# Kernel optimization log

Measured on AMD Instinct MI355X. Metric: run time of the kernel, lower is better.

The kernel has to match this reference:

```python
import jax, jax.numpy as jnp
import numpy as np
from functools import partial

D = 1024
H = 4 * D
E = 8
K_TOP = 2
B, T = 4, 2048
NEG_INF = jnp.float32(-1e30)


def setup_inputs() -> dict:
    key = jax.random.key(0)
    ks = jax.random.split(key, 12)
    s = 0.02
    return {
        "x": jax.random.normal(ks[0], (B, T, D), jnp.float32),
        "noise": jax.random.normal(ks[1], (B, T, E), jnp.float32),
        "gate_w": jax.random.normal(ks[2], (E, D), jnp.float32) * s,
        "gate_b": jnp.zeros((E,), jnp.float32),
        "var_w": jax.random.normal(ks[3], (E, D), jnp.float32) * s,
        "var_b": jnp.zeros((E,), jnp.float32),
        "w1": jax.random.normal(ks[4], (E, H, D), jnp.float32) * s,
        "b1": jnp.zeros((E, H), jnp.float32),
        "w2": jax.random.normal(ks[5], (E, D, H), jnp.float32) * s,
        "b2": jnp.zeros((E, D), jnp.float32),
    }


def reference(x, noise, gate_w, gate_b, var_w, var_b, w1, b1, w2, b2):
    # Noisy top-k gating
    logits = jnp.einsum("btd,ed->bte", x, gate_w) + gate_b          # [B,T,E]
    std = jax.nn.softplus(jnp.einsum("btd,ed->bte", x, var_w) + var_b)
    noisy = logits + noise * std                                      # [B,T,E]
    _, idx = jax.lax.top_k(noisy, K_TOP)                              # [B,T,K]
    # boolean top-k mask over experts
    mask = (idx[..., None] == jnp.arange(E)).any(axis=-2)             # [B,T,E]
    coef = jax.nn.softmax(jnp.where(mask, noisy, NEG_INF), axis=-1)   # zeros outside top-k

    # Combine: sum_e coef_e * FFN_e(x). coef is exactly 0 for non-selected
    # experts, so this equals the masked gather/scatter math. Scan over the
    # small expert dim to avoid a [E,B,T,H] intermediate.
    coef_e = jnp.moveaxis(coef, -1, 0)                                # [E,B,T]

    def body(acc, ew):
        w1e, b1e, w2e, b2e, ce = ew
        h = jax.nn.relu(jnp.einsum("btd,hd->bth", x, w1e) + b1e)
        y = jnp.einsum("bth,dh->btd", h, w2e) + b2e
        return acc + y * ce[..., None], None

    out, _ = jax.lax.scan(body, jnp.zeros_like(x), (w1, b1, w2, b2, coef_e))
    return out
```

## Files before the change

kernel.cpp:

```cpp
#include <hip/hip_runtime.h>
#include <hip/hip_bf16.h>
#include <math.h>

#define NTOK 8192
#define DD   1024
#define HH   4096
#define NE   8
#define BM 128
#define BN 128
#define BK 64
#define SLOT_CAP (2 * NTOK + NE * BM)

typedef __bf16 bf16;
typedef __bf16 bf16x8 __attribute__((ext_vector_type(8)));
typedef __bf16 bf16x4 __attribute__((ext_vector_type(4)));
typedef float  f32x4  __attribute__((ext_vector_type(4)));

typedef __attribute__((address_space(3))) unsigned char lds_u8;
typedef const __attribute__((address_space(1))) unsigned char g_u8;

__device__ __forceinline__ void gload16(const bf16* g, bf16* l) {
  __builtin_amdgcn_global_load_lds((g_u8*)g, (lds_u8*)l, 16, 0, 0);
}

__device__ __forceinline__ float softplus_f(float v) {
  return fmaxf(v, 0.f) + log1pf(expf(-fabsf(v)));
}

__global__ __launch_bounds__(64) void moe_gate_kernel(
    const float* __restrict__ x, const float* __restrict__ noise,
    const float* __restrict__ gate_w, const float* __restrict__ gate_b,
    const float* __restrict__ var_w,  const float* __restrict__ var_b,
    float* __restrict__ coef2, int* __restrict__ t2e, int* __restrict__ counts,
    bf16* __restrict__ xb)
{
  const int t = blockIdx.x;
  const int lane = threadIdx.x;
  const float* xt = x + (size_t)t * DD;
  bf16* xbt = xb + (size_t)t * DD;
  float pg[NE], pv[NE];
  #pragma unroll
  for (int e = 0; e < NE; ++e) { pg[e] = 0.f; pv[e] = 0.f; }
  #pragma unroll 4
  for (int i = 0; i < DD / 64; ++i) {
    const int d = lane + i * 64;
    const float xv = xt[d];
    xbt[d] = (bf16)xv;
    #pragma unroll
    for (int e = 0; e < NE; ++e) {
      pg[e] = fmaf(xv, gate_w[e * DD + d], pg[e]);
      pv[e] = fmaf(xv, var_w[e * DD + d], pv[e]);
    }
  }
  #pragma unroll
  for (int e = 0; e < NE; ++e) {
    #pragma unroll
    for (int off = 32; off; off >>= 1) {
      pg[e] += __shfl_xor(pg[e], off);
      pv[e] += __shfl_xor(pv[e], off);
    }
  }
  if (lane == 0) {
    float noisy[NE];
    #pragma unroll
    for (int e = 0; e < NE; ++e) {
      const float lg = pg[e] + gate_b[e];
      const float sd = softplus_f(pv[e] + var_b[e]);
      noisy[e] = lg + noise[t * NE + e] * sd;
    }
    int i1 = 0; float n1 = noisy[0];
    #pragma unroll
    for (int e = 1; e < NE; ++e) if (noisy[e] > n1) { n1 = noisy[e]; i1 = e; }
    int i2 = -1; float n2 = -3.0e38f;
    #pragma unroll
    for (int e = 0; e < NE; ++e) if (e != i1 && noisy[e] > n2) { n2 = noisy[e]; i2 = e; }
    const float e2 = expf(n2 - n1);
    const float den = 1.f + e2;
    coef2[t * 2 + 0] = 1.f / den;
    coef2[t * 2 + 1] = e2 / den;
    t2e[t * 2 + 0] = i1;
    t2e[t * 2 + 1] = i2;
    atomicAdd(&counts[i1], 1);
    atomicAdd(&counts[i2], 1);
  }
}

__global__ void moe_offsets_kernel(const int* __restrict__ counts, int* __restrict__ po) {
  if (threadIdx.x == 0) {
    int acc = 0;
    po[0] = 0;
    for (int e = 0; e < NE; ++e) {
      acc += ((counts[e] + BM - 1) / BM) * BM;
      po[e + 1] = acc;
    }
  }
}

__global__ __launch_bounds__(256) void moe_scatter_kernel(
    const int* __restrict__ t2e, const float* __restrict__ coef2,
    const int* __restrict__ po, int* __restrict__ cnt2,
    int* __restrict__ assign_tok, float* __restrict__ slot_coef)
{
  const int t = blockIdx.x * 256 + threadIdx.x;
  if (t >= NTOK) return;
  #pragma unroll
  for (int k = 0; k < 2; ++k) {
    const int e = t2e[t * 2 + k];
    const int pos = atomicAdd(&cnt2[e], 1);
    const int slot = po[e] + pos;
    assign_tok[slot] = t;
    slot_coef[slot] = coef2[t * 2 + k];
  }
}

__global__ __launch_bounds__(256) void cvt_bf16_kernel(const float* __restrict__ src,
                                                       bf16* __restrict__ dst, int n4) {
  for (int i = blockIdx.x * 256 + threadIdx.x; i < n4; i += gridDim.x * 256) {
    const float4 f = ((const float4*)src)[i];
    bf16x4 v;
    v[0] = (bf16)f.x; v[1] = (bf16)f.y; v[2] = (bf16)f.z; v[3] = (bf16)f.w;
    ((bf16x4*)dst)[i] = v;
  }
}

template<int KDIM, int NCOLS, bool FFN1>
__global__ __launch_bounds__(256) void moe_gemm_kernel(
    const bf16* __restrict__ Asrc, const bf16* __restrict__ Wsrc,
    const float* __restrict__ bias,
    const int* __restrict__ assign_tok, const float* __restrict__ slot_coef,
    const int* __restrict__ po,
    bf16* __restrict__ hout, float* __restrict__ out,
    int chunk_base, int gx)
{
  __shared__ bf16 As[BM][BK];
  __shared__ bf16 Bs[BN][BK];
  __shared__ int toks[BM];

  const int nwg = gridDim.x;
  const int lin = blockIdx.x;
  const int q = nwg >> 3, r = nwg & 7;
  const int xcd = lin & 7, idx = lin >> 3;
  const int wg = (xcd < r ? xcd * (q + 1) : r * (q + 1) + (xcd - r) * q) + idx;
  int bx, by;
  if constexpr (FFN1) { bx = wg % gx; by = wg / gx; }
  else               { by = wg % (NCOLS / BN); bx = wg / (NCOLS / BN); }

  const int po8 = po[NE];
  const int row0 = chunk_base + bx * BM;
  if (row0 >= po8) return;
  int e = 0;
  while (row0 >= po[e + 1]) ++e;
  const int bn0 = by * BN;
  const bf16* We = Wsrc + (size_t)e * ((size_t)HH * DD);
  const int tid = threadIdx.x, lane = tid & 63, wave = tid >> 6;
  if (tid < BM) toks[tid] = assign_tok[row0 + tid];
  __syncthreads();

  const int rin = lane >> 3;
  const int c8s = ((lane & 7) ^ rin) * 8;
  const bf16* asrc[4];
  const bf16* bsrc[4];
  #pragma unroll
  for (int i = 0; i < 4; ++i) {
    const int c = wave * 4 + i;
    const int row = c * 8 + rin;
    int ar;
    if constexpr (FFN1) {
      const int s = toks[row];
      ar = s < 0 ? 0 : s;
    } else {
      ar = row0 - chunk_base + row;
    }
    asrc[i] = Asrc + (size_t)ar * KDIM + c8s;
    bsrc[i] = We + (size_t)(bn0 + row) * KDIM + c8s;
  }

  const int la = lane & 15, hi = lane >> 4;
  const int wm = (wave >> 1) * 64, wn = (wave & 1) * 64;
  f32x4 acc[4][4];
  #pragma unroll
  for (int m = 0; m < 4; ++m)
    #pragma unroll
    for (int n = 0; n < 4; ++n) acc[m][n] = {0.f, 0.f, 0.f, 0.f};

  for (int k0 = 0; k0 < KDIM; k0 += BK) {
    #pragma unroll
    for (int i = 0; i < 4; ++i) gload16(asrc[i] + k0, &As[(wave * 4 + i) * 8][0]);
    #pragma unroll
    for (int i = 0; i < 4; ++i) gload16(bsrc[i] + k0, &Bs[(wave * 4 + i) * 8][0]);
    __syncthreads();
    #pragma unroll
    for (int ks = 0; ks < 2; ++ks) {
      bf16x8 af[4], bff[4];
      #pragma unroll
      for (int m = 0; m < 4; ++m) {
        const int row = wm + m * 16 + la;
        const int c8 = (ks * 4 + hi) ^ (row & 7);
        af[m] = *(const bf16x8*)(&As[row][c8 * 8]);
      }
      #pragma unroll
      for (int n = 0; n < 4; ++n) {
        const int row = wn + n * 16 + la;
        const int c8 = (ks * 4 + hi) ^ (row & 7);
        bff[n] = *(const bf16x8*)(&Bs[row][c8 * 8]);
      }
      #pragma unroll
      for (int m = 0; m < 4; ++m)
        #pragma unroll
        for (int n = 0; n < 4; ++n)
          acc[m][n] = __builtin_amdgcn_mfma_f32_16x16x32_bf16(af[m], bff[n], acc[m][n], 0, 0, 0);
    }
    __syncthreads();
  }

  if constexpr (FFN1) {
    const int hrow0 = row0 - chunk_base;
    #pragma unroll
    for (int n = 0; n < 4; ++n) {
      const int col = bn0 + wn + n * 16 + la;
      const float bb = bias[e * NCOLS + col];
      #pragma unroll
      for (int m = 0; m < 4; ++m) {
        const int rbase = wm + m * 16 + hi * 4;
        #pragma unroll
        for (int rr = 0; rr < 4; ++rr) {
          float v = acc[m][n][rr] + bb;
          v = v > 0.f ? v : 0.f;
          hout[(size_t)(hrow0 + rbase + rr) * HH + col] = (bf16)v;
        }
      }
    }
  } else {
    #pragma unroll
    for (int n = 0; n < 4; ++n) {
      const int col = bn0 + wn + n * 16 + la;
      const float bb = bias[e * NCOLS + col];
      #pragma unroll
      for (int m = 0; m < 4; ++m) {
        const int rbase = wm + m * 16 + hi * 4;
        #pragma unroll
        for (int rr = 0; rr < 4; ++rr) {
          const int trow = rbase + rr;
          const int tok = toks[trow];
          if (tok >= 0) {
            const float c = slot_coef[row0 + trow];
            atomicAdd(out + (size_t)tok * DD + col, c * (acc[m][n][rr] + bb));
          }
        }
      }
    }
  }
}

extern "C" void kernel_launch(void* const* d_in, const int* in_sizes, int n_in,
                              void* d_out, int out_size, void* d_ws, size_t ws_size,
                              hipStream_t stream) {
  const float* x      = (const float*)d_in[0];
  const float* noise  = (const float*)d_in[1];
  const float* gate_w = (const float*)d_in[2];
  const float* gate_b = (const float*)d_in[3];
  const float* var_w  = (const float*)d_in[4];
  const float* var_b  = (const float*)d_in[5];
  const float* w1     = (const float*)d_in[6];
  const float* b1     = (const float*)d_in[7];
  const float* w2     = (const float*)d_in[8];
  const float* b2     = (const float*)d_in[9];
  float* out = (float*)d_out;
  (void)in_sizes; (void)n_in; (void)out_size;

  char* ws = (char*)d_ws;
  size_t off = 0;
  auto alloc = [&](size_t bytes) {
    off = (off + 255) & ~(size_t)255;
    size_t o = off;
    off += bytes;
    return o;
  };
  bf16*  xb         = (bf16*)(ws + alloc((size_t)NTOK * DD * 2));
  float* coef2      = (float*)(ws + alloc((size_t)NTOK * 2 * 4));
  int*   t2e        = (int*)(ws + alloc((size_t)NTOK * 2 * 4));
  int*   counts     = (int*)(ws + alloc(64));
  int*   cnt2       = counts + 8;
  int*   po         = (int*)(ws + alloc(64));
  int*   assign_tok = (int*)(ws + alloc((size_t)SLOT_CAP * 4));
  float* slot_coef  = (float*)(ws + alloc((size_t)SLOT_CAP * 4));
  bf16*  w1b        = (bf16*)(ws + alloc((size_t)NE * HH * DD * 2));
  bf16*  w2b        = (bf16*)(ws + alloc((size_t)NE * DD * HH * 2));
  off = (off + 255) & ~(size_t)255;
  const size_t h_avail = ws_size > off ? ws_size - off : 0;
  int chunk_rows = (int)(h_avail / ((size_t)HH * 2));
  chunk_rows = (chunk_rows / BM) * BM;
  if (chunk_rows < BM) chunk_rows = BM;
  if (chunk_rows > SLOT_CAP) chunk_rows = SLOT_CAP;
  bf16* hbuf = (bf16*)(ws + off);

  hipMemsetAsync(counts, 0, 64, stream);
  hipMemsetAsync(assign_tok, 0xFF, (size_t)SLOT_CAP * 4, stream);
  hipMemsetAsync(out, 0, (size_t)NTOK * DD * 4, stream);

  moe_gate_kernel<<<NTOK, 64, 0, stream>>>(x, noise, gate_w, gate_b, var_w, var_b,
                                           coef2, t2e, counts, xb);
  moe_offsets_kernel<<<1, 64, 0, stream>>>(counts, po);
  moe_scatter_kernel<<<NTOK / 256, 256, 0, stream>>>(t2e, coef2, po, cnt2,
                                                     assign_tok, slot_coef);
  cvt_bf16_kernel<<<2048, 256, 0, stream>>>(w1, w1b, NE * HH * DD / 4);
  cvt_bf16_kernel<<<2048, 256, 0, stream>>>(w2, w2b, NE * DD * HH / 4);

  const int rounds = (SLOT_CAP + chunk_rows - 1) / chunk_rows;
  for (int r = 0; r < rounds; ++r) {
    const int cb = r * chunk_rows;
    const int rows_here = (cb + chunk_rows <= SLOT_CAP) ? chunk_rows : (SLOT_CAP - cb);
    const int gx = rows_here / BM;
    moe_gemm_kernel<DD, HH, true><<<gx * (HH / BN), 256, 0, stream>>>(
        xb, w1b, b1, assign_tok, slot_coef, po, hbuf, nullptr, cb, gx);
    moe_gemm_kernel<HH, DD, false><<<gx * (DD / BN), 256, 0, stream>>>(
        hbuf, w2b, b2, assign_tok, slot_coef, po, nullptr, out, cb, gx);
  }
}
```

Measured before the change: 956.6 us.

## Double-buffer LDS tiles in MoE GEMM and merge weight conversion kernels

The GEMM main loop now keeps two LDS buffers and issues the global-to-LDS loads for the next K tile before computing the current one. It waits with explicit vmcnt counters and raw barriers instead of __syncthreads, so global load latency can overlap the MFMA work. The two fp32-to-bf16 weight conversion launches are also merged into one kernel. In exchange, LDS use per block doubles, which may lower occupancy, and the hand-written waitcnt values depend on each thread having exactly 8 loads in flight per stage.

```diff
diff --git a/kernel.cpp b/kernel.cpp
--- a/kernel.cpp
+++ b/kernel.cpp
@@ -113,15 +113,23 @@
   }
 }
 
-__global__ __launch_bounds__(256) void cvt_bf16_kernel(const float* __restrict__ src,
-                                                       bf16* __restrict__ dst, int n4) {
-  for (int i = blockIdx.x * 256 + threadIdx.x; i < n4; i += gridDim.x * 256) {
-    const float4 f = ((const float4*)src)[i];
+__global__ __launch_bounds__(256) void cvt2_bf16_kernel(
+    const float* __restrict__ s1, bf16* __restrict__ d1, int n41,
+    const float* __restrict__ s2, bf16* __restrict__ d2, int n42)
+{
+  for (int i = blockIdx.x * 256 + threadIdx.x; i < n41 + n42; i += gridDim.x * 256) {
+    const float* s = (i < n41) ? s1 : s2;
+    bf16* d = (i < n41) ? d1 : d2;
+    const int j = (i < n41) ? i : i - n41;
+    const float4 f = ((const float4*)s)[j];
     bf16x4 v;
     v[0] = (bf16)f.x; v[1] = (bf16)f.y; v[2] = (bf16)f.z; v[3] = (bf16)f.w;
-    ((bf16x4*)dst)[i] = v;
-  }
-}
+    ((bf16x4*)d)[j] = v;
+  }
+}
+
+#define VMCNT8 asm volatile("s_waitcnt vmcnt(8)" ::: "memory")
+#define VMCNT0 asm volatile("s_waitcnt vmcnt(0)" ::: "memory")
 
 template<int KDIM, int NCOLS, bool FFN1>
 __global__ __launch_bounds__(256) void moe_gemm_kernel(
@@ -132,8 +140,9 @@
     bf16* __restrict__ hout, float* __restrict__ out,
     int chunk_base, int gx)
 {
-  __shared__ bf16 As[BM][BK];
-  __shared__ bf16 Bs[BN][BK];
+  constexpr int NK = KDIM / BK;
+  __shared__ bf16 As[2][BM][BK];
+  __shared__ bf16 Bs[2][BN][BK];
   __shared__ int toks[BM];
 
   const int nwg = gridDim.x;
@@ -175,6 +184,14 @@
     bsrc[i] = We + (size_t)(bn0 + row) * KDIM + c8s;
   }
 
+  auto stage = [&](int sel, int kt) {
+    const int k0 = kt * BK;
+    #pragma unroll
+    for (int i = 0; i < 4; ++i) gload16(asrc[i] + k0, &As[sel][(wave * 4 + i) * 8][0]);
+    #pragma unroll
+    for (int i = 0; i < 4; ++i) gload16(bsrc[i] + k0, &Bs[sel][(wave * 4 + i) * 8][0]);
+  };
+
   const int la = lane & 15, hi = lane >> 4;
   const int wm = (wave >> 1) * 64, wn = (wave & 1) * 64;
   f32x4 acc[4][4];
@@ -183,12 +200,18 @@
     #pragma unroll
     for (int n = 0; n < 4; ++n) acc[m][n] = {0.f, 0.f, 0.f, 0.f};
 
-  for (int k0 = 0; k0 < KDIM; k0 += BK) {
-    #pragma unroll
-    for (int i = 0; i < 4; ++i) gload16(asrc[i] + k0, &As[(wave * 4 + i) * 8][0]);
-    #pragma unroll
-    for (int i = 0; i < 4; ++i) gload16(bsrc[i] + k0, &Bs[(wave * 4 + i) * 8][0]);
-    __syncthreads();
+  stage(0, 0);
+
+  for (int kt = 0; kt < NK; ++kt) {
+    const int b = kt & 1;
+    if (kt + 1 < NK) {
+      stage(b ^ 1, kt + 1);
+      VMCNT8;
+    } else {
+      VMCNT0;
+    }
+    __builtin_amdgcn_s_barrier();
+
     #pragma unroll
     for (int ks = 0; ks < 2; ++ks) {
       bf16x8 af[4], bff[4];
@@ -196,13 +219,13 @@
       for (int m = 0; m < 4; ++m) {
         const int row = wm + m * 16 + la;
         const int c8 = (ks * 4 + hi) ^ (row & 7);
-        af[m] = *(const bf16x8*)(&As[row][c8 * 8]);
+        af[m] = *(const bf16x8*)(&As[b][row][c8 * 8]);
       }
       #pragma unroll
       for (int n = 0; n < 4; ++n) {
         const int row = wn + n * 16 + la;
         const int c8 = (ks * 4 + hi) ^ (row & 7);
-        bff[n] = *(const bf16x8*)(&Bs[row][c8 * 8]);
+        bff[n] = *(const bf16x8*)(&Bs[b][row][c8 * 8]);
       }
       #pragma unroll
       for (int m = 0; m < 4; ++m)
@@ -210,7 +233,7 @@
         for (int n = 0; n < 4; ++n)
           acc[m][n] = __builtin_amdgcn_mfma_f32_16x16x32_bf16(af[m], bff[n], acc[m][n], 0, 0, 0);
     }
-    __syncthreads();
+    __builtin_amdgcn_s_barrier();
   }
 
   if constexpr (FFN1) {
@@ -303,8 +326,8 @@
   moe_offsets_kernel<<<1, 64, 0, stream>>>(counts, po);
   moe_scatter_kernel<<<NTOK / 256, 256, 0, stream>>>(t2e, coef2, po, cnt2,
                                                      assign_tok, slot_coef);
-  cvt_bf16_kernel<<<2048, 256, 0, stream>>>(w1, w1b, NE * HH * DD / 4);
-  cvt_bf16_kernel<<<2048, 256, 0, stream>>>(w2, w2b, NE * DD * HH / 4);
+  cvt2_bf16_kernel<<<2048, 256, 0, stream>>>(w1, w1b, NE * HH * DD / 4,
+                                             w2, w2b, NE * DD * HH / 4);
 
   const int rounds = (SLOT_CAP + chunk_rows - 1) / chunk_rows;
   for (int r = 0; r < rounds; ++r) {
```

New measurement: 953.0 us. No clear change (-0.4%).
